# Optimization experiments

Measured on AMD Instinct MI355X. Metric: run time of the kernel, lower is better.

## Reference

```python
import jax, jax.numpy as jnp
import numpy as np

# Dims: B=2, S=2048, D=1024 hidden, E=8 experts, F=2752 ffn (SwiGLU), top-1 gate,
# capacity_factor=1.0 -> capacity C = (B*S)//E = 512. Residual-MoE (moe_use_residual=True).

def setup_inputs() -> dict:
    key = jax.random.key(0)
    ks = jax.random.split(key, 10)
    B, S, D, E, F = 2, 2048, 1024, 8, 2752
    sc = 0.02
    return {
        "hidden_states": jax.random.normal(ks[0], (B, S, D), jnp.float32),
        "wg":  jax.random.normal(ks[1], (D, E), jnp.float32) * sc,   # gate
        "w1":  jax.random.normal(ks[2], (E, D, F), jnp.float32) * sc,  # expert SwiGLU
        "w3":  jax.random.normal(ks[3], (E, D, F), jnp.float32) * sc,
        "w2":  jax.random.normal(ks[4], (E, F, D), jnp.float32) * sc,
        "rw1": jax.random.normal(ks[5], (D, F), jnp.float32) * sc,    # residual MLP (SwiGLU, no bias)
        "rw3": jax.random.normal(ks[6], (D, F), jnp.float32) * sc,
        "rw2": jax.random.normal(ks[7], (F, D), jnp.float32) * sc,
        "cw":  jax.random.normal(ks[8], (D, 2), jnp.float32) * sc,    # coefficient Linear(D, 2)
        "cb":  jnp.zeros((2,), jnp.float32),
    }


def _moe_forward(x, wg, w1, w3, w2):
    """GShard/DeepSpeed-style top-1 gated MoE with capacity + token dropping.
    x: [T, D] flattened tokens. Returns (out [T,D], l_aux scalar, exp_counts [E])."""
    T, D = x.shape
    E = wg.shape[1]
    C = max(4, T // E)  # capacity_factor = 1.0, min_capacity = 4

    logits = x @ wg                                  # [T, E]
    gates = jax.nn.softmax(logits, axis=-1)
    idx = jnp.argmax(gates, axis=-1)                 # top-1 expert per token
    mask1 = jax.nn.one_hot(idx, E, dtype=gates.dtype)  # [T, E]
    exp_counts = jnp.sum(mask1, axis=0).astype(jnp.int32)

    # load-balancing aux loss (DeepSpeed top1gating)
    me = jnp.mean(gates, axis=0)
    ce = jnp.mean(mask1, axis=0)
    l_aux = jnp.sum(me * ce) * E

    # position of each token within its expert's buffer; drop overflow
    locations = jnp.cumsum(mask1, axis=0) - 1.0      # [T, E]
    mask1 = mask1 * (locations < C)
    loc_s = jnp.sum(locations * mask1, axis=1).astype(jnp.int32)  # [T]
    gates1 = jnp.sum(gates * mask1, axis=1)          # [T] gate weight (0 if dropped)

    loc_oh = jax.nn.one_hot(loc_s, C, dtype=gates.dtype)          # [T, C]
    combine = gates1[:, None, None] * mask1[:, :, None] * loc_oh[:, None, :]  # [T, E, C]
    dispatch = (combine > 0).astype(x.dtype)

    xe = jnp.einsum("tec,td->ecd", dispatch, x)      # dispatch to [E, C, D]
    h = jax.nn.silu(jnp.einsum("ecd,edf->ecf", xe, w1)) * jnp.einsum("ecd,edf->ecf", xe, w3)
    ye = jnp.einsum("ecf,efd->ecd", h, w2)           # expert SwiGLU FFN
    out = jnp.einsum("tec,ecd->td", combine, ye)     # weighted combine back to tokens
    return out, l_aux, exp_counts


def reference(hidden_states, wg, w1, w3, w2, rw1, rw3, rw2, cw, cb):
    B, S, D = hidden_states.shape
    x = hidden_states.reshape(-1, D)
    moe_out, l_aux, exp_counts = _moe_forward(x, wg, w1, w3, w2)
    moe_out = moe_out.reshape(B, S, D)

    # residual SwiGLU MLP + softmax-gated combine (Residual-MoE)
    mlp = (jax.nn.silu(hidden_states @ rw1) * (hidden_states @ rw3)) @ rw2
    coef = jax.nn.softmax(hidden_states @ cw + cb, axis=-1)  # [B, S, 2]
    output = moe_out * coef[..., 0:1] + mlp * coef[..., 1:2]
    return output, l_aux, exp_counts
```

## Files before the change

kernel.cpp:

```cpp
#include <hip/hip_runtime.h>
#include <hip/hip_bf16.h>
#include <stdint.h>

#define T_TOK 4096
#define DD 1024
#define EE 8
#define CC 512
#define FF 2752
#define FP 2816

typedef __attribute__((ext_vector_type(8))) short bf16x8;
typedef __attribute__((ext_vector_type(4))) float f32x4;
typedef __attribute__((ext_vector_type(4))) unsigned short us4;
typedef __attribute__((ext_vector_type(8))) unsigned short us8;

__device__ __forceinline__ float bf2f(unsigned short u) {
  union { float f; unsigned int i; } v; v.i = ((unsigned int)u) << 16; return v.f;
}
__device__ __forceinline__ unsigned short f2bf(float f) {
  union { float f; unsigned int i; } v; v.f = f;
  unsigned int r = v.i + 0x7fffu + ((v.i >> 16) & 1u);
  return (unsigned short)(r >> 16);
}

#define GLDS16(g, l) __builtin_amdgcn_global_load_lds( \
    (const __attribute__((address_space(1))) void*)(g), \
    (__attribute__((address_space(3))) void*)(l), 16, 0, 0)

#define STG_CHUNK(l) (((l & 3) ^ ((l >> 3) & 3)) * 8)
#define RD_OFF(fr, fq) ((fr) * 32 + (((fq) ^ (((fr) >> 1) & 3)) * 8))

#define BAR() do { asm volatile("" ::: "memory"); __builtin_amdgcn_s_barrier(); \
                   asm volatile("" ::: "memory"); } while (0)

template<int RT>
__global__ __launch_bounds__(256)
void transpose_k(const float* __restrict__ in, const float* __restrict__ in2,
                 unsigned short* __restrict__ out, unsigned short* __restrict__ out2,
                 int R, int C, long inStride, long outStride) {
  __shared__ unsigned short sm[RT * 64];
  int b = blockIdx.z;
  if (b < EE) { in += (long)b * inStride; out += (long)b * outStride; }
  else { in = in2; out = out2; }
  int cb = blockIdx.x * 64, rb = blockIdx.y * RT;
  int t = threadIdx.x;
  int rr = t >> 4, c4 = (t & 15) * 4;
#pragma unroll
  for (int i = 0; i < RT / 16; ++i) {
    int r = rr + i * 16;
    float4 v = *(const float4*)(in + (long)(rb + r) * C + cb + c4);
    us4 o; o.x = f2bf(v.x); o.y = f2bf(v.y); o.z = f2bf(v.z); o.w = f2bf(v.w);
    *(us4*)&sm[r * 64 + (c4 ^ (((r >> 3) & 7) << 3))] = o;
  }
  __syncthreads();
#pragma unroll
  for (int j = 0; j < (64 * (RT / 8)) / 256; ++j) {
    int idx = t + j * 256;
    int g, c;
    if (RT == 128) { g = idx & 15; c = idx >> 4; }
    else           { g = idx & 7;  c = idx >> 3; }
    int r8 = g * 8;
    us8 o;
#pragma unroll
    for (int k = 0; k < 8; ++k) {
      int r = r8 + k;
      o[k] = sm[r * 64 + (c ^ (((r >> 3) & 7) << 3))];
    }
    *(us8*)(out + (long)(cb + c) * R + rb + r8) = o;
  }
}

__global__ void zero_me_k(float* me) { if (threadIdx.x < EE) me[threadIdx.x] = 0.0f; }

__global__ void gate_k(const float* __restrict__ x, const float* __restrict__ wg,
                       const float* __restrict__ cw, const float* __restrict__ cbv,
                       int* __restrict__ idx, float* __restrict__ gatev,
                       float* __restrict__ coef, float* __restrict__ me_sum) {
  int tid = threadIdx.x, lane = tid & 63, wv = tid >> 6;
  int t = blockIdx.x * 4 + wv;
  const float* xr = x + (long)t * DD;
  float acc[EE] = {0,0,0,0,0,0,0,0};
  float c0 = 0.0f, c1 = 0.0f;
  for (int d = lane; d < DD; d += 64) {
    float xv = xr[d];
#pragma unroll
    for (int e = 0; e < EE; ++e) acc[e] += xv * wg[d * EE + e];
    c0 += xv * cw[d * 2 + 0];
    c1 += xv * cw[d * 2 + 1];
  }
#pragma unroll
  for (int o = 32; o > 0; o >>= 1) {
#pragma unroll
    for (int e = 0; e < EE; ++e) acc[e] += __shfl_xor(acc[e], o);
    c0 += __shfl_xor(c0, o);
    c1 += __shfl_xor(c1, o);
  }
  __shared__ float sme[EE];
  if (tid < EE) sme[tid] = 0.0f;
  __syncthreads();
  if (lane == 0) {
    float m = acc[0]; int am = 0;
#pragma unroll
    for (int e = 1; e < EE; ++e) if (acc[e] > m) { m = acc[e]; am = e; }
    float g[EE]; float s = 0.0f;
#pragma unroll
    for (int e = 0; e < EE; ++e) { g[e] = __expf(acc[e] - m); s += g[e]; }
    float inv = 1.0f / s;
    idx[t] = am;
    gatev[t] = g[am] * inv;
#pragma unroll
    for (int e = 0; e < EE; ++e) atomicAdd(&sme[e], g[e] * inv);
    float l0 = c0 + cbv[0], l1 = c1 + cbv[1];
    float mm = fmaxf(l0, l1);
    float e0 = __expf(l0 - mm), e1 = __expf(l1 - mm);
    float is = 1.0f / (e0 + e1);
    coef[t * 2 + 0] = e0 * is;
    coef[t * 2 + 1] = e1 * is;
  }
  __syncthreads();
  if (tid < EE) atomicAdd(&me_sum[tid], sme[tid]);
}

__global__ void scan_k(const int* __restrict__ idx, const float* __restrict__ me_sum,
                       int* __restrict__ slot, int* __restrict__ tok,
                       float* __restrict__ out_tail) {
  __shared__ int sidx[T_TOK];
  __shared__ int counts[EE];
  int tid = threadIdx.x;
  for (int i = tid; i < T_TOK; i += 512) sidx[i] = idx[i];
  __syncthreads();
  int e = tid >> 6, lane = tid & 63;
  int base = 0;
  for (int it = 0; it < T_TOK / 64; ++it) {
    int t = it * 64 + lane;
    bool f = (sidx[t] == e);
    unsigned long long m = __ballot(f);
    if (f) {
      int loc = base + __popcll(m & ((1ull << lane) - 1ull));
      slot[t] = (loc < CC) ? loc : -1;
      if (loc < CC) tok[e * CC + loc] = t;
    }
    base += __popcll(m);
  }
  if (lane == 0) counts[e] = base;
  __syncthreads();
  int filled = min(counts[e], CC);
  for (int c = filled + lane; c < CC; c += 64) tok[e * CC + c] = -1;
  if (tid == 0) {
    float la = 0.0f;
    for (int i = 0; i < EE; ++i) la += me_sum[i] * (float)counts[i];
    la *= (float)EE / ((float)T_TOK * (float)T_TOK);
    out_tail[0] = la;
    for (int i = 0; i < EE; ++i) out_tail[1 + i] = (float)counts[i];
  }
}

__global__ void gather_k(const float* __restrict__ x, const int* __restrict__ tok,
                         unsigned short* __restrict__ xb, unsigned short* __restrict__ xe) {
  int r = blockIdx.x, tid = threadIdx.x;
  int d = tid * 4;
  if (r < T_TOK) {
    float4 v = *(const float4*)(x + (long)r * DD + d);
    us4 o; o.x = f2bf(v.x); o.y = f2bf(v.y); o.z = f2bf(v.z); o.w = f2bf(v.w);
    *(us4*)(xb + (long)r * DD + d) = o;
  } else {
    int s = r - T_TOK;
    int t = tok[s];
    us4 o = {0, 0, 0, 0};
    if (t >= 0) {
      float4 v = *(const float4*)(x + (long)t * DD + d);
      o.x = f2bf(v.x); o.y = f2bf(v.y); o.z = f2bf(v.z); o.w = f2bf(v.w);
    }
    *(us4*)(xe + (long)s * DD + d) = o;
  }
}

__global__ __launch_bounds__(512, 2)
void gemm1_k(const unsigned short* __restrict__ xcat,
             const unsigned short* __restrict__ w1t, const unsigned short* __restrict__ w3t,
             const unsigned short* __restrict__ rw1t, const unsigned short* __restrict__ rw3t,
             unsigned short* __restrict__ Hcat) {
  int lin = blockIdx.x;
  int work = (lin & 7) * 88 + (lin >> 3);
  int mtile, ntile;
  if (work < 352) {
    int e = work / 44, r = work - e * 44;
    ntile = r >> 1;
    mtile = e * 2 + (r & 1);
  } else {
    int q = work - 352;
    ntile = q >> 4;
    mtile = 16 + (q & 15);
  }
  const unsigned short* A = xcat + (size_t)mtile * 256 * DD;
  const unsigned short *B1, *B3;
  if (mtile < 16) { int e = mtile >> 1; B1 = w1t + (size_t)e * FP * DD; B3 = w3t + (size_t)e * FP * DD; }
  else { B1 = rw1t; B3 = rw3t; }
  unsigned short* H = Hcat + (size_t)mtile * 256 * FF;
  int n0 = ntile * 128;

  __shared__ __align__(16) unsigned short lds[65536];
  char* Lc = (char*)lds;

  int tid = threadIdx.x, l = tid & 63, w = tid >> 6;
  int wm = w >> 1, wn = w & 1;
  int fr = l & 15, fq = l >> 4;
  int srow = l >> 2, soff = STG_CHUNK(l);
  int rdo = RD_OFF(fr, fq);

  const unsigned short* gA0 = A + (size_t)(w * 16 + srow) * DD + soff;
  const unsigned short* gA1 = A + (size_t)((8 + w) * 16 + srow) * DD + soff;
  const unsigned short* gB1 = B1 + (size_t)(n0 + w * 16 + srow) * DD + soff;
  const unsigned short* gB3 = B3 + (size_t)(n0 + w * 16 + srow) * DD + soff;

#define STG_A1(bb, kk) do {                                        \
    GLDS16(gA0 + (kk), Lc + (bb) * 16384 + w * 1024);              \
    GLDS16(gA1 + (kk), Lc + (bb) * 16384 + (8 + w) * 1024); } while (0)
#define STG_B1(bb, kk) do {                                        \
    GLDS16(gB1 + (kk), Lc + 65536 + (bb) * 8192 + w * 1024);       \
    GLDS16(gB3 + (kk), Lc + 98304 + (bb) * 8192 + w * 1024); } while (0)

  f32x4 acc1[4][4] = {};
  f32x4 acc3[4][4] = {};

  const int HN = 32;
#pragma unroll
  for (int hh = 0; hh < 3; ++hh) { STG_A1(hh, hh * 32); STG_B1(hh, hh * 32); }
  asm volatile("s_waitcnt vmcnt(8)" ::: "memory");
  BAR();

#pragma unroll 4
  for (int h = 0; h < HN; ++h) {
    int b = h & 3;
    int hw = h + 3; if (hw >= HN) hw -= HN;
    int bn = hw & 3;
    int kk = hw * 32;
    bf16x8 af[4], b1f[4], b3f[4];

#pragma unroll
    for (int mi = 0; mi < 4; ++mi)
      af[mi] = *(const bf16x8*)(lds + b * 8192 + (wm * 4 + mi) * 512 + rdo);
#pragma unroll
    for (int ni = 0; ni < 4; ++ni)
      b1f[ni] = *(const bf16x8*)(lds + 32768 + b * 4096 + (wn * 4 + ni) * 512 + rdo);
    STG_A1(bn, kk);
    BAR();
    __builtin_amdgcn_s_setprio(1);
#pragma unroll
    for (int mi = 0; mi < 4; ++mi)
#pragma unroll
      for (int ni = 0; ni < 4; ++ni)
        acc1[mi][ni] = __builtin_amdgcn_mfma_f32_16x16x32_bf16(af[mi], b1f[ni], acc1[mi][ni], 0, 0, 0);
    __builtin_amdgcn_s_setprio(0);
    BAR();

#pragma unroll
    for (int ni = 0; ni < 4; ++ni)
      b3f[ni] = *(const bf16x8*)(lds + 49152 + b * 4096 + (wn * 4 + ni) * 512 + rdo);
    STG_B1(bn, kk);
    asm volatile("s_waitcnt vmcnt(8)" ::: "memory");
    BAR();
    __builtin_amdgcn_s_setprio(1);
#pragma unroll
    for (int mi = 0; mi < 4; ++mi)
#pragma unroll
      for (int ni = 0; ni < 4; ++ni)
        acc3[mi][ni] = __builtin_amdgcn_mfma_f32_16x16x32_bf16(af[mi], b3f[ni], acc3[mi][ni], 0, 0, 0);
    __builtin_amdgcn_s_setprio(0);
    BAR();
  }
#undef STG_A1
#undef STG_B1

#pragma unroll
  for (int mi = 0; mi < 4; ++mi)
#pragma unroll
    for (int ni = 0; ni < 4; ++ni)
#pragma unroll
      for (int r = 0; r < 4; ++r) {
        int gm = wm * 64 + mi * 16 + fq * 4 + r;
        int gn = n0 + wn * 64 + ni * 16 + fr;
        if (gn < FF) {
          float v1 = acc1[mi][ni][r], v3 = acc3[mi][ni][r];
          float h = v1 / (1.0f + __expf(-v1)) * v3;
          H[(size_t)gm * FF + gn] = f2bf(h);
        }
      }
}

__global__ __launch_bounds__(512, 2)
void gemm2_k(const unsigned short* __restrict__ Hcat,
             const unsigned short* __restrict__ w2t, const unsigned short* __restrict__ rw2t,
             unsigned short* __restrict__ Ycat) {
  int lin = blockIdx.x;
  int work = (lin & 7) * 32 + (lin >> 3);
  int mtile, ntile;
  if (work < 128) {
    int e = work >> 4, r = work & 15;
    ntile = r >> 1;
    mtile = e * 2 + (r & 1);
  } else {
    int q = work - 128;
    ntile = q >> 4;
    mtile = 16 + (q & 15);
  }
  const unsigned short* A = Hcat + (size_t)mtile * 256 * FF;
  const unsigned short* B = (mtile < 16) ? (w2t + (size_t)(mtile >> 1) * DD * FF) : rw2t;
  unsigned short* Y = Ycat + (size_t)mtile * 256 * DD;
  int n0 = ntile * 128;

  __shared__ __align__(16) unsigned short lds[73728];
  char* Lc = (char*)lds;

  int tid = threadIdx.x, l = tid & 63, w = tid >> 6;
  int wm = w >> 1, wn = w & 1;
  int fr = l & 15, fq = l >> 4;
  int srow = l >> 2, soff = STG_CHUNK(l);
  int rdo = RD_OFF(fr, fq);

  const unsigned short* gA0 = A + (size_t)(w * 16 + srow) * FF + soff;
  const unsigned short* gA1 = A + (size_t)((8 + w) * 16 + srow) * FF + soff;
  const unsigned short* gB  = B + (size_t)(n0 + w * 16 + srow) * FF + soff;

#define STG2(bb, kk) do {                                          \
    GLDS16(gA0 + (kk), Lc + (bb) * 16384 + w * 1024);              \
    GLDS16(gA1 + (kk), Lc + (bb) * 16384 + (8 + w) * 1024);        \
    GLDS16(gB  + (kk), Lc + 98304 + (bb) * 8192 + w * 1024); } while (0)

  f32x4 acc[4][4] = {};

  const int HN = 86;
#pragma unroll
  for (int hh = 0; hh < 5; ++hh) STG2(hh, hh * 32);
  asm volatile("s_waitcnt vmcnt(12)" ::: "memory");
  BAR();

  int b = 0;
#pragma unroll 2
  for (int h = 0; h < HN; ++h) {
    int bn = b ? b - 1 : 5;
    int hw = h + 5; if (hw >= HN) hw -= HN;
    int kk = hw * 32;
    bf16x8 af[4], bf[4];

#pragma unroll
    for (int mi = 0; mi < 4; ++mi)
      af[mi] = *(const bf16x8*)(lds + b * 8192 + (wm * 4 + mi) * 512 + rdo);
#pragma unroll
    for (int ni = 0; ni < 4; ++ni)
      bf[ni] = *(const bf16x8*)(lds + 49152 + b * 4096 + (wn * 4 + ni) * 512 + rdo);
    STG2(bn, kk);
    asm volatile("s_waitcnt vmcnt(12)" ::: "memory");
    BAR();
    __builtin_amdgcn_s_setprio(1);
#pragma unroll
    for (int mi = 0; mi < 4; ++mi)
#pragma unroll
      for (int ni = 0; ni < 4; ++ni)
        acc[mi][ni] = __builtin_amdgcn_mfma_f32_16x16x32_bf16(af[mi], bf[ni], acc[mi][ni], 0, 0, 0);
    __builtin_amdgcn_s_setprio(0);
    BAR();

    ++b; if (b == 6) b = 0;
  }
#undef STG2

#pragma unroll
  for (int mi = 0; mi < 4; ++mi)
#pragma unroll
    for (int ni = 0; ni < 4; ++ni)
#pragma unroll
      for (int r = 0; r < 4; ++r) {
        int gm = wm * 64 + mi * 16 + fq * 4 + r;
        int gn = n0 + wn * 64 + ni * 16 + fr;
        Y[(size_t)gm * DD + gn] = f2bf(acc[mi][ni][r]);
      }
}

__global__ void combine_k(const unsigned short* __restrict__ Ye, const unsigned short* __restrict__ Yr,
                          const int* __restrict__ idx, const int* __restrict__ slot,
                          const float* __restrict__ gatev, const float* __restrict__ coef,
                          float* __restrict__ out) {
  int t = blockIdx.x, tid = threadIdx.x;
  int d = tid * 4;
  float c0 = coef[t * 2], c1 = coef[t * 2 + 1];
  int s = slot[t];
  float g = gatev[t] * c0;
  us4 vr = *(const us4*)(Yr + (size_t)t * DD + d);
  float4 o;
  if (s >= 0) {
    us4 ve = *(const us4*)(Ye + ((size_t)idx[t] * CC + s) * DD + d);
    o.x = g * bf2f(ve.x) + c1 * bf2f(vr.x);
    o.y = g * bf2f(ve.y) + c1 * bf2f(vr.y);
    o.z = g * bf2f(ve.z) + c1 * bf2f(vr.z);
    o.w = g * bf2f(ve.w) + c1 * bf2f(vr.w);
  } else {
    o.x = c1 * bf2f(vr.x);
    o.y = c1 * bf2f(vr.y);
    o.z = c1 * bf2f(vr.z);
    o.w = c1 * bf2f(vr.w);
  }
  *(float4*)(out + (size_t)t * DD + d) = o;
}

extern "C" void kernel_launch(void* const* d_in, const int* in_sizes, int n_in,
                              void* d_out, int out_size, void* d_ws, size_t ws_size,
                              hipStream_t stream) {
  const float* x   = (const float*)d_in[0];
  const float* wg  = (const float*)d_in[1];
  const float* w1  = (const float*)d_in[2];
  const float* w3  = (const float*)d_in[3];
  const float* w2  = (const float*)d_in[4];
  const float* rw1 = (const float*)d_in[5];
  const float* rw3 = (const float*)d_in[6];
  const float* rw2 = (const float*)d_in[7];
  const float* cw  = (const float*)d_in[8];
  const float* cbv = (const float*)d_in[9];
  float* out = (float*)d_out;

  char* ws = (char*)d_ws;
  size_t o = 0;
  auto alloc = [&](size_t bytes) -> char* {
    char* p = ws + o; o = (o + bytes + 255) & ~(size_t)255; return p;
  };
  unsigned short* w1t  = (unsigned short*)alloc((size_t)EE * FP * DD * 2);
  unsigned short* w3t  = (unsigned short*)alloc((size_t)EE * FP * DD * 2);
  unsigned short* w2t  = (unsigned short*)alloc((size_t)EE * DD * FF * 2);
  unsigned short* rw1t = (unsigned short*)alloc((size_t)FP * DD * 2);
  unsigned short* rw3t = (unsigned short*)alloc((size_t)FP * DD * 2);
  unsigned short* rw2t = (unsigned short*)alloc((size_t)DD * FF * 2);
  unsigned short* xe   = (unsigned short*)alloc((size_t)T_TOK * DD * 2);
  unsigned short* xb   = (unsigned short*)alloc((size_t)T_TOK * DD * 2);
  unsigned short* He   = (unsigned short*)alloc((size_t)T_TOK * FF * 2);
  unsigned short* Hr   = (unsigned short*)alloc((size_t)T_TOK * FF * 2);
  unsigned short* Ye   = (unsigned short*)alloc((size_t)T_TOK * DD * 2);
  unsigned short* Yr   = (unsigned short*)alloc((size_t)T_TOK * DD * 2);
  int*   idxp  = (int*)alloc(T_TOK * 4);
  float* gatev = (float*)alloc(T_TOK * 4);
  int*   slotp = (int*)alloc(T_TOK * 4);
  int*   tokp  = (int*)alloc(EE * CC * 4);
  float* coefp = (float*)alloc(T_TOK * 2 * 4);
  float* mep   = (float*)alloc(256);
  if (o > ws_size) return;

  transpose_k<128><<<dim3(43, 8, EE + 1), 256, 0, stream>>>(w1, rw1, w1t, rw1t, DD, FF, (long)DD * FF, (long)FP * DD);
  transpose_k<128><<<dim3(43, 8, EE + 1), 256, 0, stream>>>(w3, rw3, w3t, rw3t, DD, FF, (long)DD * FF, (long)FP * DD);
  transpose_k<64><<<dim3(16, 43, EE + 1), 256, 0, stream>>>(w2, rw2, w2t, rw2t, FF, DD, (long)FF * DD, (long)DD * FF);

  zero_me_k<<<1, 64, 0, stream>>>(mep);
  gate_k<<<T_TOK / 4, 256, 0, stream>>>(x, wg, cw, cbv, idxp, gatev, coefp, mep);
  scan_k<<<1, 512, 0, stream>>>(idxp, mep, slotp, tokp, out + (size_t)T_TOK * DD);
  gather_k<<<2 * T_TOK, 256, 0, stream>>>(x, tokp, xb, xe);
  gemm1_k<<<704, 512, 0, stream>>>(xe, w1t, w3t, rw1t, rw3t, He);
  gemm2_k<<<256, 512, 0, stream>>>(He, w2t, rw2t, Ye);
  combine_k<<<T_TOK, 256, 0, stream>>>(Ye, Yr, idxp, slotp, gatev, coefp, out);
}
```

Baseline: 303.2 us.

## Load fp32 w1/w3 directly in gemm1, converting to bf16 in registers, dropping transposes

The two transpose/convert kernels for w1/w3 (and rw1/rw3) are removed. gemm1 now streams the original fp32 [D,F] weights straight into LDS with a swizzled layout, then converts them to bf16 with v_cvt_pk_bf16_f32 before the MFMAs. The pipeline becomes a 3-stage ring with one barrier per k-step. This avoids writing and re-reading about 90MB of bf16 copies, but gemm1 now reads twice the weight bytes per tile, uses 144KB of LDS (which may limit occupancy below the launch-bounds target of 2), and adds conversion ALU work.

```diff
diff --git a/kernel.cpp b/kernel.cpp
--- a/kernel.cpp
+++ b/kernel.cpp
@@ -7,7 +7,6 @@
 #define EE 8
 #define CC 512
 #define FF 2752
-#define FP 2816
 
 typedef __attribute__((ext_vector_type(8))) short bf16x8;
 typedef __attribute__((ext_vector_type(4))) float f32x4;
@@ -177,8 +176,8 @@
 
 __global__ __launch_bounds__(512, 2)
 void gemm1_k(const unsigned short* __restrict__ xcat,
-             const unsigned short* __restrict__ w1t, const unsigned short* __restrict__ w3t,
-             const unsigned short* __restrict__ rw1t, const unsigned short* __restrict__ rw3t,
+             const float* __restrict__ w1, const float* __restrict__ w3,
+             const float* __restrict__ rw1, const float* __restrict__ rw3,
              unsigned short* __restrict__ Hcat) {
   int lin = blockIdx.x;
   int work = (lin & 7) * 88 + (lin >> 3);
@@ -193,14 +192,14 @@
     mtile = 16 + (q & 15);
   }
   const unsigned short* A = xcat + (size_t)mtile * 256 * DD;
-  const unsigned short *B1, *B3;
-  if (mtile < 16) { int e = mtile >> 1; B1 = w1t + (size_t)e * FP * DD; B3 = w3t + (size_t)e * FP * DD; }
-  else { B1 = rw1t; B3 = rw3t; }
+  const float *B1, *B3;
+  if (mtile < 16) { int e = mtile >> 1; B1 = w1 + (size_t)e * DD * FF; B3 = w3 + (size_t)e * DD * FF; }
+  else { B1 = rw1; B3 = rw3; }
   unsigned short* H = Hcat + (size_t)mtile * 256 * FF;
   int n0 = ntile * 128;
 
-  __shared__ __align__(16) unsigned short lds[65536];
-  char* Lc = (char*)lds;
+  __shared__ __align__(16) char Lc[147456];
+  const unsigned short* ldsS = (const unsigned short*)Lc;
 
   int tid = threadIdx.x, l = tid & 63, w = tid >> 6;
   int wm = w >> 1, wn = w & 1;
@@ -210,67 +209,96 @@
 
   const unsigned short* gA0 = A + (size_t)(w * 16 + srow) * DD + soff;
   const unsigned short* gA1 = A + (size_t)((8 + w) * 16 + srow) * DD + soff;
-  const unsigned short* gB1 = B1 + (size_t)(n0 + w * 16 + srow) * DD + soff;
-  const unsigned short* gB3 = B3 + (size_t)(n0 + w * 16 + srow) * DD + soff;
-
-#define STG_A1(bb, kk) do {                                        \
-    GLDS16(gA0 + (kk), Lc + (bb) * 16384 + w * 1024);              \
-    GLDS16(gA1 + (kk), Lc + (bb) * 16384 + (8 + w) * 1024); } while (0)
-#define STG_B1(bb, kk) do {                                        \
-    GLDS16(gB1 + (kk), Lc + 65536 + (bb) * 8192 + w * 1024);       \
-    GLDS16(gB3 + (kk), Lc + 98304 + (bb) * 8192 + w * 1024); } while (0)
+  int lrow = l >> 5;
+  int kl0 = 2 * w + lrow;
+  int kl1 = 16 + 2 * w + lrow;
+  int cs0 = (l & 31) ^ (((kl0 >> 3) & 1) << 2);
+  int cs1 = (l & 31) ^ (((kl1 >> 3) & 1) << 2);
+  int nn0 = n0 + 4 * cs0; if (nn0 >= FF) nn0 = 0;
+  int nn1 = n0 + 4 * cs1; if (nn1 >= FF) nn1 = 0;
+  const float* gB1a = B1 + (size_t)kl0 * FF + nn0;
+  const float* gB1b = B1 + (size_t)kl1 * FF + nn1;
+  const float* gB3a = B3 + (size_t)kl0 * FF + nn0;
+  const float* gB3b = B3 + (size_t)kl1 * FF + nn1;
+
+  int cb[4];
+#pragma unroll
+  for (int ni = 0; ni < 4; ++ni)
+    cb[ni] = fq * 4096 + ((((wn * 4 + ni) * 64 + fr * 4)) ^ ((fq & 1) << 6));
+
+#define STG1(bb, hw) do { size_t ka = (size_t)(hw) * 32; size_t kb = ka * FF;   \
+    GLDS16(gA0 + ka, Lc + (bb) * 16384 + w * 1024);                             \
+    GLDS16(gA1 + ka, Lc + (bb) * 16384 + (8 + w) * 1024);                       \
+    GLDS16(gB1a + kb, Lc + 49152 + (bb) * 16384 + w * 1024);                    \
+    GLDS16(gB1b + kb, Lc + 49152 + (bb) * 16384 + (8 + w) * 1024);              \
+    GLDS16(gB3a + kb, Lc + 98304 + (bb) * 16384 + w * 1024);                    \
+    GLDS16(gB3b + kb, Lc + 98304 + (bb) * 16384 + (8 + w) * 1024); } while (0)
 
   f32x4 acc1[4][4] = {};
   f32x4 acc3[4][4] = {};
 
   const int HN = 32;
-#pragma unroll
-  for (int hh = 0; hh < 3; ++hh) { STG_A1(hh, hh * 32); STG_B1(hh, hh * 32); }
-  asm volatile("s_waitcnt vmcnt(8)" ::: "memory");
-  BAR();
-
-#pragma unroll 4
+  STG1(0, 0);
+  STG1(1, 1);
+
   for (int h = 0; h < HN; ++h) {
-    int b = h & 3;
-    int hw = h + 3; if (hw >= HN) hw -= HN;
-    int bn = hw & 3;
-    int kk = hw * 32;
-    bf16x8 af[4], b1f[4], b3f[4];
-
+    int buf = h % 3;
+    int hw = h + 2; if (hw >= HN) hw -= HN;
+    int bufw = (buf + 2) % 3;
+
+    asm volatile("s_waitcnt vmcnt(6)" ::: "memory");
+    BAR();
+    STG1(bufw, hw);
+
+    const char* Bb1 = Lc + 49152 + buf * 16384;
+    const char* Bb3 = Lc + 98304 + buf * 16384;
+    bf16x8 af[4];
 #pragma unroll
     for (int mi = 0; mi < 4; ++mi)
-      af[mi] = *(const bf16x8*)(lds + b * 8192 + (wm * 4 + mi) * 512 + rdo);
-#pragma unroll
-    for (int ni = 0; ni < 4; ++ni)
-      b1f[ni] = *(const bf16x8*)(lds + 32768 + b * 4096 + (wn * 4 + ni) * 512 + rdo);
-    STG_A1(bn, kk);
-    BAR();
-    __builtin_amdgcn_s_setprio(1);
-#pragma unroll
-    for (int mi = 0; mi < 4; ++mi)
+      af[mi] = *(const bf16x8*)(ldsS + buf * 8192 + (wm * 4 + mi) * 512 + rdo);
+
+    {
+      float fb[4][8];
 #pragma unroll
       for (int ni = 0; ni < 4; ++ni)
-        acc1[mi][ni] = __builtin_amdgcn_mfma_f32_16x16x32_bf16(af[mi], b1f[ni], acc1[mi][ni], 0, 0, 0);
-    __builtin_amdgcn_s_setprio(0);
-    BAR();
-
-#pragma unroll
-    for (int ni = 0; ni < 4; ++ni)
-      b3f[ni] = *(const bf16x8*)(lds + 49152 + b * 4096 + (wn * 4 + ni) * 512 + rdo);
-    STG_B1(bn, kk);
-    asm volatile("s_waitcnt vmcnt(8)" ::: "memory");
-    BAR();
-    __builtin_amdgcn_s_setprio(1);
-#pragma unroll
-    for (int mi = 0; mi < 4; ++mi)
+#pragma unroll
+        for (int j = 0; j < 8; ++j)
+          fb[ni][j] = *(const float*)(Bb1 + cb[ni] + j * 512);
+      __builtin_amdgcn_s_setprio(1);
+#pragma unroll
+      for (int ni = 0; ni < 4; ++ni) {
+        union { bf16x8 h; unsigned int u[4]; } bu;
+#pragma unroll
+        for (int p = 0; p < 4; ++p)
+          asm("v_cvt_pk_bf16_f32 %0, %1, %2" : "=v"(bu.u[p]) : "v"(fb[ni][2 * p]), "v"(fb[ni][2 * p + 1]));
+#pragma unroll
+        for (int mi = 0; mi < 4; ++mi)
+          acc1[mi][ni] = __builtin_amdgcn_mfma_f32_16x16x32_bf16(af[mi], bu.h, acc1[mi][ni], 0, 0, 0);
+      }
+      __builtin_amdgcn_s_setprio(0);
+    }
+    {
+      float fb[4][8];
 #pragma unroll
       for (int ni = 0; ni < 4; ++ni)
-        acc3[mi][ni] = __builtin_amdgcn_mfma_f32_16x16x32_bf16(af[mi], b3f[ni], acc3[mi][ni], 0, 0, 0);
-    __builtin_amdgcn_s_setprio(0);
-    BAR();
-  }
-#undef STG_A1
-#undef STG_B1
+#pragma unroll
+        for (int j = 0; j < 8; ++j)
+          fb[ni][j] = *(const float*)(Bb3 + cb[ni] + j * 512);
+      __builtin_amdgcn_s_setprio(1);
+#pragma unroll
+      for (int ni = 0; ni < 4; ++ni) {
+        union { bf16x8 h; unsigned int u[4]; } bu;
+#pragma unroll
+        for (int p = 0; p < 4; ++p)
+          asm("v_cvt_pk_bf16_f32 %0, %1, %2" : "=v"(bu.u[p]) : "v"(fb[ni][2 * p]), "v"(fb[ni][2 * p + 1]));
+#pragma unroll
+        for (int mi = 0; mi < 4; ++mi)
+          acc3[mi][ni] = __builtin_amdgcn_mfma_f32_16x16x32_bf16(af[mi], bu.h, acc3[mi][ni], 0, 0, 0);
+      }
+      __builtin_amdgcn_s_setprio(0);
+    }
+  }
+#undef STG1
 
 #pragma unroll
   for (int mi = 0; mi < 4; ++mi)
@@ -305,7 +333,7 @@
     mtile = 16 + (q & 15);
   }
   const unsigned short* A = Hcat + (size_t)mtile * 256 * FF;
-  const unsigned short* B = (mtile < 16) ? (w2t + (size_t)(mtile >> 1) * DD * FF) : rw2t;
+  const unsigned short* B = (mtile < 16) ? (w2t + (size_t)(mtile >> 1) * (size_t)DD * FF) : rw2t;
   unsigned short* Y = Ycat + (size_t)mtile * 256 * DD;
   int n0 = ntile * 128;
 
@@ -423,11 +451,7 @@
   auto alloc = [&](size_t bytes) -> char* {
     char* p = ws + o; o = (o + bytes + 255) & ~(size_t)255; return p;
   };
-  unsigned short* w1t  = (unsigned short*)alloc((size_t)EE * FP * DD * 2);
-  unsigned short* w3t  = (unsigned short*)alloc((size_t)EE * FP * DD * 2);
   unsigned short* w2t  = (unsigned short*)alloc((size_t)EE * DD * FF * 2);
-  unsigned short* rw1t = (unsigned short*)alloc((size_t)FP * DD * 2);
-  unsigned short* rw3t = (unsigned short*)alloc((size_t)FP * DD * 2);
   unsigned short* rw2t = (unsigned short*)alloc((size_t)DD * FF * 2);
   unsigned short* xe   = (unsigned short*)alloc((size_t)T_TOK * DD * 2);
   unsigned short* xb   = (unsigned short*)alloc((size_t)T_TOK * DD * 2);
@@ -443,15 +467,13 @@
   float* mep   = (float*)alloc(256);
   if (o > ws_size) return;
 
-  transpose_k<128><<<dim3(43, 8, EE + 1), 256, 0, stream>>>(w1, rw1, w1t, rw1t, DD, FF, (long)DD * FF, (long)FP * DD);
-  transpose_k<128><<<dim3(43, 8, EE + 1), 256, 0, stream>>>(w3, rw3, w3t, rw3t, DD, FF, (long)DD * FF, (long)FP * DD);
   transpose_k<64><<<dim3(16, 43, EE + 1), 256, 0, stream>>>(w2, rw2, w2t, rw2t, FF, DD, (long)FF * DD, (long)DD * FF);
 
   zero_me_k<<<1, 64, 0, stream>>>(mep);
   gate_k<<<T_TOK / 4, 256, 0, stream>>>(x, wg, cw, cbv, idxp, gatev, coefp, mep);
   scan_k<<<1, 512, 0, stream>>>(idxp, mep, slotp, tokp, out + (size_t)T_TOK * DD);
   gather_k<<<2 * T_TOK, 256, 0, stream>>>(x, tokp, xb, xe);
-  gemm1_k<<<704, 512, 0, stream>>>(xe, w1t, w3t, rw1t, rw3t, He);
+  gemm1_k<<<704, 512, 0, stream>>>(xe, w1, w3, rw1, rw3, He);
   gemm2_k<<<256, 512, 0, stream>>>(He, w2t, rw2t, Ye);
   combine_k<<<T_TOK, 256, 0, stream>>>(Ye, Yr, idxp, slotp, gatev, coefp, out);
 }
```

Result: faster. 271.4 us (-10.5%).
